# Performance work log

Measured on AMD Instinct MI355X. Metric: run time of the kernel, lower is better.

Reference implementation:

```python
import jax, jax.numpy as jnp
import numpy as np

IN_F, HID, OUT = 768, 64, 1
BATCH = 131072
NNZ1 = int(0.1 * IN_F * HID)   # 4915
NNZ2 = int(0.1 * HID * HID)    # 409
NNZ3 = int(0.5 * HID * OUT)    # 32


def _coo(key, nnz, n_rows, n_cols):
    kr, kc, kv = jax.random.split(key, 3)
    rows = jax.random.randint(kr, (nnz,), 0, n_rows, dtype=jnp.int32)
    cols = jax.random.randint(kc, (nnz,), 0, n_cols, dtype=jnp.int32)
    vals = jax.random.normal(kv, (nnz,), dtype=jnp.float32)
    return jnp.stack([rows, cols]), vals


def setup_inputs() -> dict:
    key = jax.random.key(0)
    kx, k1, k2, k3, kb1, kb2, kb3 = jax.random.split(key, 7)
    x = jax.random.normal(kx, (BATCH, IN_F), dtype=jnp.float32)
    idx1, val1 = _coo(k1, NNZ1, IN_F, HID)
    idx2, val2 = _coo(k2, NNZ2, HID, HID)
    idx3, val3 = _coo(k3, NNZ3, HID, OUT)
    b1 = jax.random.normal(kb1, (HID,), dtype=jnp.float32)
    b2 = jax.random.normal(kb2, (HID,), dtype=jnp.float32)
    b3 = jax.random.normal(kb3, (OUT,), dtype=jnp.float32)
    return {"x": x, "idx1": idx1, "val1": val1, "b1": b1,
            "idx2": idx2, "val2": val2, "b2": b2,
            "idx3": idx3, "val3": val3, "b3": b3}


def _densify(idx, vals, shape):
    # COO -> dense; duplicate indices accumulate (torch coalesce semantics)
    return jnp.zeros(shape, dtype=vals.dtype).at[idx[0], idx[1]].add(vals)


def reference(x, idx1, val1, b1, idx2, val2, b2, idx3, val3, b3):
    x = x.reshape(x.shape[0], -1)                      # [B, IN_F]
    W1 = _densify(idx1, val1, (IN_F, HID))
    W2 = _densify(idx2, val2, (HID, HID))
    W3 = _densify(idx3, val3, (HID, OUT))
    h = jax.nn.relu(x @ W1 + b1)                       # [B, 64]
    h = jax.nn.relu(h @ W2 + b2)                       # [B, 64]
    return h @ W3 + b3                                 # [B, 1]
```

## Files before the change

kernel.cpp:

```cpp
#include <hip/hip_runtime.h>
#include <cstdint>
#include <cstddef>

#define IN_F 768
#define HID  64
#define NNZ1 4915
#define NNZ2 409
#define NNZ3 32
#define BATCH 131072

#define OFF_W1D 0u
#define OFF_W2D 196608u
#define OFF_W3D 212992u
#define OFF_W1F 213248u
#define OFF_W2F 311552u
#define WS_NEED 319744u

typedef __bf16 bf16x8 __attribute__((ext_vector_type(8)));
typedef float  f32x4  __attribute__((ext_vector_type(4)));

union FragU { bf16x8 v; uint32_t u[4]; uint4 q; };

__device__ __forceinline__ uint32_t f2bf1(float f) {
    uint32_t u = __float_as_uint(f);
    return (u + 0x7FFFu + ((u >> 16) & 1u)) >> 16;
}
__device__ __forceinline__ uint32_t f2bf2(float lo, float hi) {
    uint32_t a = __float_as_uint(lo);
    uint32_t b = __float_as_uint(hi);
    a = a + 0x7FFFu + ((a >> 16) & 1u);
    b = b + 0x7FFFu + ((b >> 16) & 1u);
    return (a >> 16) | (b & 0xFFFF0000u);
}

__global__ void scatter_coo(const int* __restrict__ idx1, const float* __restrict__ val1,
                            const int* __restrict__ idx2, const float* __restrict__ val2,
                            const int* __restrict__ idx3, const float* __restrict__ val3,
                            float* __restrict__ W1d, float* __restrict__ W2d,
                            float* __restrict__ W3d) {
    int t = blockIdx.x * blockDim.x + threadIdx.x;
    if (t < NNZ1) {
        int r = idx1[t], c = idx1[NNZ1 + t];
        atomicAdd(&W1d[r * HID + c], val1[t]);
    } else if (t < NNZ1 + NNZ2) {
        int i = t - NNZ1;
        int r = idx2[i], c = idx2[NNZ2 + i];
        atomicAdd(&W2d[r * HID + c], val2[i]);
    } else if (t < NNZ1 + NNZ2 + NNZ3) {
        int i = t - NNZ1 - NNZ2;
        int r = idx3[i], c = idx3[NNZ3 + i];
        atomicAdd(&W3d[r * 1 + c], val3[i]);
    }
}

__global__ void frag_build(const float* __restrict__ W1d, const float* __restrict__ W2d,
                           uint4* __restrict__ W1f, uint4* __restrict__ W2f) {
    int t = blockIdx.x * blockDim.x + threadIdx.x;
    const int n1 = 24 * 4 * 64;
    const int n2 = 2 * 4 * 64;
    if (t < n1) {
        int lane = t & 63;
        int fi = t >> 6;
        int kstep = fi >> 2, nt = fi & 3;
        int m = lane & 15, quad = lane >> 4;
        uint32_t u[4];
#pragma unroll
        for (int jj = 0; jj < 4; ++jj) {
            int k = kstep * 32 + quad * 8 + jj * 2;
            u[jj] = f2bf2(W1d[k * HID + nt * 16 + m], W1d[(k + 1) * HID + nt * 16 + m]);
        }
        W1f[t] = make_uint4(u[0], u[1], u[2], u[3]);
    } else if (t < n1 + n2) {
        int tt = t - n1;
        int lane = tt & 63;
        int fi = tt >> 6;
        int kstep = fi >> 2, nt = fi & 3;
        int m = lane & 15, quad = lane >> 4;
        uint32_t u[4];
#pragma unroll
        for (int jj = 0; jj < 4; ++jj) {
            int k = kstep * 32 + quad * 8 + jj * 2;
            u[jj] = f2bf2(W2d[k * HID + nt * 16 + m], W2d[(k + 1) * HID + nt * 16 + m]);
        }
        W2f[tt] = make_uint4(u[0], u[1], u[2], u[3]);
    }
}

__global__ __launch_bounds__(256) void mlp_fused(
    const float* __restrict__ x,
    const uint4* __restrict__ W1f,
    const uint4* __restrict__ W2f,
    const float* __restrict__ W3d,
    const float* __restrict__ b1,
    const float* __restrict__ b2,
    const float* __restrict__ b3,
    float* __restrict__ out)
{
    __shared__ __align__(16) uint16_t h1s[4][16][72];

    const int lane = threadIdx.x & 63;
    const int w    = threadIdx.x >> 6;
    const int m    = lane & 15;
    const int quad = lane >> 4;
    const int rowbase = blockIdx.x * 64 + w * 16;

    f32x4 acc[4] = {{0,0,0,0},{0,0,0,0},{0,0,0,0},{0,0,0,0}};

    const float* xr = x + (size_t)(rowbase + m) * IN_F + quad * 8;
    const uint4* w1p = W1f + lane;

#pragma unroll 2
    for (int k = 0; k < 24; ++k) {
        const float4 xa = *(const float4*)(xr + k * 32);
        const float4 xb = *(const float4*)(xr + k * 32 + 4);
        FragU a;
        a.u[0] = f2bf2(xa.x, xa.y);
        a.u[1] = f2bf2(xa.z, xa.w);
        a.u[2] = f2bf2(xb.x, xb.y);
        a.u[3] = f2bf2(xb.z, xb.w);
        FragU b0, b1f, b2f, b3f;
        b0.q  = w1p[(k * 4 + 0) * 64];
        b1f.q = w1p[(k * 4 + 1) * 64];
        b2f.q = w1p[(k * 4 + 2) * 64];
        b3f.q = w1p[(k * 4 + 3) * 64];
        acc[0] = __builtin_amdgcn_mfma_f32_16x16x32_bf16(a.v, b0.v,  acc[0], 0, 0, 0);
        acc[1] = __builtin_amdgcn_mfma_f32_16x16x32_bf16(a.v, b1f.v, acc[1], 0, 0, 0);
        acc[2] = __builtin_amdgcn_mfma_f32_16x16x32_bf16(a.v, b2f.v, acc[2], 0, 0, 0);
        acc[3] = __builtin_amdgcn_mfma_f32_16x16x32_bf16(a.v, b3f.v, acc[3], 0, 0, 0);
    }

#pragma unroll
    for (int nt = 0; nt < 4; ++nt) {
        const int col = nt * 16 + m;
        const float bias = b1[col];
#pragma unroll
        for (int r = 0; r < 4; ++r) {
            float h = acc[nt][r] + bias;
            h = h > 0.f ? h : 0.f;
            h1s[w][quad * 4 + r][col] = (uint16_t)f2bf1(h);
        }
    }

    f32x4 acc2[4] = {{0,0,0,0},{0,0,0,0},{0,0,0,0},{0,0,0,0}};
#pragma unroll
    for (int k2 = 0; k2 < 2; ++k2) {
        FragU a2;
        a2.q = *(const uint4*)&h1s[w][m][k2 * 32 + quad * 8];
#pragma unroll
        for (int nt = 0; nt < 4; ++nt) {
            FragU bb; bb.q = W2f[(k2 * 4 + nt) * 64 + lane];
            acc2[nt] = __builtin_amdgcn_mfma_f32_16x16x32_bf16(a2.v, bb.v, acc2[nt], 0, 0, 0);
        }
    }

    float w3v[4];
#pragma unroll
    for (int nt = 0; nt < 4; ++nt) w3v[nt] = W3d[nt * 16 + m];

    float p[4] = {0.f, 0.f, 0.f, 0.f};
#pragma unroll
    for (int nt = 0; nt < 4; ++nt) {
        const float bias = b2[nt * 16 + m];
#pragma unroll
        for (int r = 0; r < 4; ++r) {
            float h = acc2[nt][r] + bias;
            h = h > 0.f ? h : 0.f;
            p[r] += h * w3v[nt];
        }
    }
#pragma unroll
    for (int off = 1; off < 16; off <<= 1) {
#pragma unroll
        for (int r = 0; r < 4; ++r) p[r] += __shfl_xor(p[r], off, 16);
    }
    const float bb3 = b3[0];
    if (m == 0) {
#pragma unroll
        for (int r = 0; r < 4; ++r) out[rowbase + quad * 4 + r] = p[r] + bb3;
    }
}

extern "C" void kernel_launch(void* const* d_in, const int* in_sizes, int n_in,
                              void* d_out, int out_size, void* d_ws, size_t ws_size,
                              hipStream_t stream) {
    const float* x    = (const float*)d_in[0];
    const int*   idx1 = (const int*)  d_in[1];
    const float* val1 = (const float*)d_in[2];
    const float* b1   = (const float*)d_in[3];
    const int*   idx2 = (const int*)  d_in[4];
    const float* val2 = (const float*)d_in[5];
    const float* b2   = (const float*)d_in[6];
    const int*   idx3 = (const int*)  d_in[7];
    const float* val3 = (const float*)d_in[8];
    const float* b3   = (const float*)d_in[9];
    float* out = (float*)d_out;

    char* ws = (char*)d_ws;
    float* W1d = (float*)(ws + OFF_W1D);
    float* W2d = (float*)(ws + OFF_W2D);
    float* W3d = (float*)(ws + OFF_W3D);
    uint4* W1f = (uint4*)(ws + OFF_W1F);
    uint4* W2f = (uint4*)(ws + OFF_W2F);

    hipMemsetAsync(d_ws, 0, OFF_W1F, stream);

    const int nnz_total = NNZ1 + NNZ2 + NNZ3;
    scatter_coo<<<(nnz_total + 255) / 256, 256, 0, stream>>>(
        idx1, val1, idx2, val2, idx3, val3, W1d, W2d, W3d);

    const int nfrag = 24 * 4 * 64 + 2 * 4 * 64;
    frag_build<<<(nfrag + 255) / 256, 256, 0, stream>>>(W1d, W2d, W1f, W2f);

    mlp_fused<<<BATCH / 64, 256, 0, stream>>>(x, W1f, W2f, W3d, b1, b2, b3, out);
}
```

Before: 555.9 us.

## Process 32 rows per wave with two-step register prefetch of x and W1

Each wave now computes two 16-row tiles, sharing each W1 fragment across both to halve weight loads per row. x and W1 fragments are loaded two k-steps ahead into double-buffered registers to hide global memory latency. The fp32-to-bf16 packing uses a vector convert builtin instead of manual rounding. Register use rises and the grid halves, which may reduce occupancy.

```diff
diff --git a/kernel.cpp b/kernel.cpp
--- a/kernel.cpp
+++ b/kernel.cpp
@@ -18,8 +18,10 @@
 
 typedef __bf16 bf16x8 __attribute__((ext_vector_type(8)));
 typedef float  f32x4  __attribute__((ext_vector_type(4)));
+typedef float  f32x8  __attribute__((ext_vector_type(8)));
 
 union FragU { bf16x8 v; uint32_t u[4]; uint4 q; };
+union F8U   { float4 f4[2]; f32x8 v8; };
 
 __device__ __forceinline__ uint32_t f2bf1(float f) {
     uint32_t u = __float_as_uint(f);
@@ -31,6 +33,11 @@
     a = a + 0x7FFFu + ((a >> 16) & 1u);
     b = b + 0x7FFFu + ((b >> 16) & 1u);
     return (a >> 16) | (b & 0xFFFF0000u);
+}
+
+__device__ __forceinline__ bf16x8 pack8(float4 a, float4 b) {
+    F8U u; u.f4[0] = a; u.f4[1] = b;
+    return __builtin_convertvector(u.v8, bf16x8);
 }
 
 __global__ void scatter_coo(const int* __restrict__ idx1, const float* __restrict__ val1,
@@ -86,7 +93,7 @@
     }
 }
 
-__global__ __launch_bounds__(256) void mlp_fused(
+__global__ __launch_bounds__(256, 4) void mlp_fused(
     const float* __restrict__ x,
     const uint4* __restrict__ W1f,
     const uint4* __restrict__ W2f,
@@ -96,37 +103,61 @@
     const float* __restrict__ b3,
     float* __restrict__ out)
 {
-    __shared__ __align__(16) uint16_t h1s[4][16][72];
+    __shared__ __align__(16) uint16_t h1s[4][32][72];
 
     const int lane = threadIdx.x & 63;
     const int w    = threadIdx.x >> 6;
     const int m    = lane & 15;
     const int quad = lane >> 4;
-    const int rowbase = blockIdx.x * 64 + w * 16;
-
-    f32x4 acc[4] = {{0,0,0,0},{0,0,0,0},{0,0,0,0},{0,0,0,0}};
-
-    const float* xr = x + (size_t)(rowbase + m) * IN_F + quad * 8;
+    const int rowbase = blockIdx.x * 128 + w * 32;
+
+    f32x4 acc0[4] = {{0,0,0,0},{0,0,0,0},{0,0,0,0},{0,0,0,0}};
+    f32x4 acc1[4] = {{0,0,0,0},{0,0,0,0},{0,0,0,0},{0,0,0,0}};
+
+    const float* xr0 = x + (size_t)(rowbase + m) * IN_F + quad * 8;
+    const float* xr1 = xr0 + (size_t)16 * IN_F;
     const uint4* w1p = W1f + lane;
+
+    float4 xa[2][4];
+    uint4  bq[2][4];
+
+#pragma unroll
+    for (int kk = 0; kk < 2; ++kk) {
+        xa[kk][0] = *(const float4*)(xr0 + kk * 32);
+        xa[kk][1] = *(const float4*)(xr0 + kk * 32 + 4);
+        xa[kk][2] = *(const float4*)(xr1 + kk * 32);
+        xa[kk][3] = *(const float4*)(xr1 + kk * 32 + 4);
+#pragma unroll
+        for (int nt = 0; nt < 4; ++nt) bq[kk][nt] = w1p[(kk * 4 + nt) * 64];
+    }
 
 #pragma unroll 2
     for (int k = 0; k < 24; ++k) {
-        const float4 xa = *(const float4*)(xr + k * 32);
-        const float4 xb = *(const float4*)(xr + k * 32 + 4);
-        FragU a;
-        a.u[0] = f2bf2(xa.x, xa.y);
-        a.u[1] = f2bf2(xa.z, xa.w);
-        a.u[2] = f2bf2(xb.x, xb.y);
-        a.u[3] = f2bf2(xb.z, xb.w);
+        const int cb = k & 1;
+        const float4 x0a = xa[cb][0], x0b = xa[cb][1];
+        const float4 x1a = xa[cb][2], x1b = xa[cb][3];
         FragU b0, b1f, b2f, b3f;
-        b0.q  = w1p[(k * 4 + 0) * 64];
-        b1f.q = w1p[(k * 4 + 1) * 64];
-        b2f.q = w1p[(k * 4 + 2) * 64];
-        b3f.q = w1p[(k * 4 + 3) * 64];
-        acc[0] = __builtin_amdgcn_mfma_f32_16x16x32_bf16(a.v, b0.v,  acc[0], 0, 0, 0);
-        acc[1] = __builtin_amdgcn_mfma_f32_16x16x32_bf16(a.v, b1f.v, acc[1], 0, 0, 0);
-        acc[2] = __builtin_amdgcn_mfma_f32_16x16x32_bf16(a.v, b2f.v, acc[2], 0, 0, 0);
-        acc[3] = __builtin_amdgcn_mfma_f32_16x16x32_bf16(a.v, b3f.v, acc[3], 0, 0, 0);
+        b0.q = bq[cb][0]; b1f.q = bq[cb][1]; b2f.q = bq[cb][2]; b3f.q = bq[cb][3];
+        if (k < 22) {
+            const int kn = k + 2;
+            xa[cb][0] = *(const float4*)(xr0 + kn * 32);
+            xa[cb][1] = *(const float4*)(xr0 + kn * 32 + 4);
+            xa[cb][2] = *(const float4*)(xr1 + kn * 32);
+            xa[cb][3] = *(const float4*)(xr1 + kn * 32 + 4);
+#pragma unroll
+            for (int nt = 0; nt < 4; ++nt) bq[cb][nt] = w1p[(kn * 4 + nt) * 64];
+        }
+        FragU a0, a1;
+        a0.v = pack8(x0a, x0b);
+        a1.v = pack8(x1a, x1b);
+        acc0[0] = __builtin_amdgcn_mfma_f32_16x16x32_bf16(a0.v, b0.v,  acc0[0], 0, 0, 0);
+        acc0[1] = __builtin_amdgcn_mfma_f32_16x16x32_bf16(a0.v, b1f.v, acc0[1], 0, 0, 0);
+        acc0[2] = __builtin_amdgcn_mfma_f32_16x16x32_bf16(a0.v, b2f.v, acc0[2], 0, 0, 0);
+        acc0[3] = __builtin_amdgcn_mfma_f32_16x16x32_bf16(a0.v, b3f.v, acc0[3], 0, 0, 0);
+        acc1[0] = __builtin_amdgcn_mfma_f32_16x16x32_bf16(a1.v, b0.v,  acc1[0], 0, 0, 0);
+        acc1[1] = __builtin_amdgcn_mfma_f32_16x16x32_bf16(a1.v, b1f.v, acc1[1], 0, 0, 0);
+        acc1[2] = __builtin_amdgcn_mfma_f32_16x16x32_bf16(a1.v, b2f.v, acc1[2], 0, 0, 0);
+        acc1[3] = __builtin_amdgcn_mfma_f32_16x16x32_bf16(a1.v, b3f.v, acc1[3], 0, 0, 0);
     }
 
 #pragma unroll
@@ -135,21 +166,27 @@
         const float bias = b1[col];
 #pragma unroll
         for (int r = 0; r < 4; ++r) {
-            float h = acc[nt][r] + bias;
-            h = h > 0.f ? h : 0.f;
-            h1s[w][quad * 4 + r][col] = (uint16_t)f2bf1(h);
-        }
-    }
-
-    f32x4 acc2[4] = {{0,0,0,0},{0,0,0,0},{0,0,0,0},{0,0,0,0}};
+            float h0 = acc0[nt][r] + bias;
+            h0 = h0 > 0.f ? h0 : 0.f;
+            h1s[w][quad * 4 + r][col] = (uint16_t)f2bf1(h0);
+            float h1 = acc1[nt][r] + bias;
+            h1 = h1 > 0.f ? h1 : 0.f;
+            h1s[w][16 + quad * 4 + r][col] = (uint16_t)f2bf1(h1);
+        }
+    }
+
+    f32x4 acc20[4] = {{0,0,0,0},{0,0,0,0},{0,0,0,0},{0,0,0,0}};
+    f32x4 acc21[4] = {{0,0,0,0},{0,0,0,0},{0,0,0,0},{0,0,0,0}};
 #pragma unroll
     for (int k2 = 0; k2 < 2; ++k2) {
-        FragU a2;
-        a2.q = *(const uint4*)&h1s[w][m][k2 * 32 + quad * 8];
+        FragU a20, a21;
+        a20.q = *(const uint4*)&h1s[w][m][k2 * 32 + quad * 8];
+        a21.q = *(const uint4*)&h1s[w][16 + m][k2 * 32 + quad * 8];
 #pragma unroll
         for (int nt = 0; nt < 4; ++nt) {
             FragU bb; bb.q = W2f[(k2 * 4 + nt) * 64 + lane];
-            acc2[nt] = __builtin_amdgcn_mfma_f32_16x16x32_bf16(a2.v, bb.v, acc2[nt], 0, 0, 0);
+            acc20[nt] = __builtin_amdgcn_mfma_f32_16x16x32_bf16(a20.v, bb.v, acc20[nt], 0, 0, 0);
+            acc21[nt] = __builtin_amdgcn_mfma_f32_16x16x32_bf16(a21.v, bb.v, acc21[nt], 0, 0, 0);
         }
     }
 
@@ -157,26 +194,36 @@
 #pragma unroll
     for (int nt = 0; nt < 4; ++nt) w3v[nt] = W3d[nt * 16 + m];
 
-    float p[4] = {0.f, 0.f, 0.f, 0.f};
+    float p0[4] = {0.f, 0.f, 0.f, 0.f};
+    float p1[4] = {0.f, 0.f, 0.f, 0.f};
 #pragma unroll
     for (int nt = 0; nt < 4; ++nt) {
         const float bias = b2[nt * 16 + m];
 #pragma unroll
         for (int r = 0; r < 4; ++r) {
-            float h = acc2[nt][r] + bias;
-            h = h > 0.f ? h : 0.f;
-            p[r] += h * w3v[nt];
+            float h0 = acc20[nt][r] + bias;
+            h0 = h0 > 0.f ? h0 : 0.f;
+            p0[r] += h0 * w3v[nt];
+            float h1 = acc21[nt][r] + bias;
+            h1 = h1 > 0.f ? h1 : 0.f;
+            p1[r] += h1 * w3v[nt];
         }
     }
 #pragma unroll
     for (int off = 1; off < 16; off <<= 1) {
 #pragma unroll
-        for (int r = 0; r < 4; ++r) p[r] += __shfl_xor(p[r], off, 16);
+        for (int r = 0; r < 4; ++r) {
+            p0[r] += __shfl_xor(p0[r], off, 16);
+            p1[r] += __shfl_xor(p1[r], off, 16);
+        }
     }
     const float bb3 = b3[0];
     if (m == 0) {
 #pragma unroll
-        for (int r = 0; r < 4; ++r) out[rowbase + quad * 4 + r] = p[r] + bb3;
+        for (int r = 0; r < 4; ++r) {
+            out[rowbase + quad * 4 + r] = p0[r] + bb3;
+            out[rowbase + 16 + quad * 4 + r] = p1[r] + bb3;
+        }
     }
 }
 
@@ -211,5 +258,5 @@
     const int nfrag = 24 * 4 * 64 + 2 * 4 * 64;
     frag_build<<<(nfrag + 255) / 256, 256, 0, stream>>>(W1d, W2d, W1f, W2f);
 
-    mlp_fused<<<BATCH / 64, 256, 0, stream>>>(x, W1f, W2f, W3d, b1, b2, b3, out);
-}
+    mlp_fused<<<BATCH / 128, 256, 0, stream>>>(x, W1f, W2f, W3d, b1, b2, b3, out);
+}
```

Result: slower. 598.0 us (+7.6%).

## Software-pipeline x loads with 64-wide K windows and permuted W1 fragments

Applied to the files above, without the earlier changes.

Each lane now loads 16 contiguous floats (64 bytes) of its x row per 64-wide K window, and two windows are prefetched into registers ahead of use. W1 fragments are rebuilt with a permuted K ordering so the split of each lane's 16 values into two bf16x8 A fragments matches the B fragments. The manual rounding is replaced by a vector convertvector to bf16. This aims to hide global-load latency in this memory-bound kernel and widen accesses, at the cost of more registers for the double-buffered x values and eight B fragments.

```diff
diff --git a/kernel.cpp b/kernel.cpp
--- a/kernel.cpp
+++ b/kernel.cpp
@@ -18,8 +18,10 @@
 
 typedef __bf16 bf16x8 __attribute__((ext_vector_type(8)));
 typedef float  f32x4  __attribute__((ext_vector_type(4)));
+typedef float  f32x8  __attribute__((ext_vector_type(8)));
 
 union FragU { bf16x8 v; uint32_t u[4]; uint4 q; };
+union F8U   { float4 f4[2]; f32x8 v8; };
 
 __device__ __forceinline__ uint32_t f2bf1(float f) {
     uint32_t u = __float_as_uint(f);
@@ -31,6 +33,11 @@
     a = a + 0x7FFFu + ((a >> 16) & 1u);
     b = b + 0x7FFFu + ((b >> 16) & 1u);
     return (a >> 16) | (b & 0xFFFF0000u);
+}
+
+__device__ __forceinline__ bf16x8 pack8(float4 a, float4 b) {
+    F8U u; u.f4[0] = a; u.f4[1] = b;
+    return __builtin_convertvector(u.v8, bf16x8);
 }
 
 __global__ void scatter_coo(const int* __restrict__ idx1, const float* __restrict__ val1,
@@ -63,10 +70,11 @@
         int fi = t >> 6;
         int kstep = fi >> 2, nt = fi & 3;
         int m = lane & 15, quad = lane >> 4;
+        int kbase = (kstep >> 1) * 64 + quad * 16 + (kstep & 1) * 8;
         uint32_t u[4];
 #pragma unroll
         for (int jj = 0; jj < 4; ++jj) {
-            int k = kstep * 32 + quad * 8 + jj * 2;
+            int k = kbase + jj * 2;
             u[jj] = f2bf2(W1d[k * HID + nt * 16 + m], W1d[(k + 1) * HID + nt * 16 + m]);
         }
         W1f[t] = make_uint4(u[0], u[1], u[2], u[3]);
@@ -106,27 +114,42 @@
 
     f32x4 acc[4] = {{0,0,0,0},{0,0,0,0},{0,0,0,0},{0,0,0,0}};
 
-    const float* xr = x + (size_t)(rowbase + m) * IN_F + quad * 8;
+    const float* xr = x + (size_t)(rowbase + m) * IN_F + quad * 16;
     const uint4* w1p = W1f + lane;
 
+    float4 xw[2][4];
+#pragma unroll
+    for (int i = 0; i < 4; ++i) {
+        xw[0][i] = *(const float4*)(xr + 0 * 64 + i * 4);
+        xw[1][i] = *(const float4*)(xr + 1 * 64 + i * 4);
+    }
+
 #pragma unroll 2
-    for (int k = 0; k < 24; ++k) {
-        const float4 xa = *(const float4*)(xr + k * 32);
-        const float4 xb = *(const float4*)(xr + k * 32 + 4);
-        FragU a;
-        a.u[0] = f2bf2(xa.x, xa.y);
-        a.u[1] = f2bf2(xa.z, xa.w);
-        a.u[2] = f2bf2(xb.x, xb.y);
-        a.u[3] = f2bf2(xb.z, xb.w);
-        FragU b0, b1f, b2f, b3f;
-        b0.q  = w1p[(k * 4 + 0) * 64];
-        b1f.q = w1p[(k * 4 + 1) * 64];
-        b2f.q = w1p[(k * 4 + 2) * 64];
-        b3f.q = w1p[(k * 4 + 3) * 64];
-        acc[0] = __builtin_amdgcn_mfma_f32_16x16x32_bf16(a.v, b0.v,  acc[0], 0, 0, 0);
-        acc[1] = __builtin_amdgcn_mfma_f32_16x16x32_bf16(a.v, b1f.v, acc[1], 0, 0, 0);
-        acc[2] = __builtin_amdgcn_mfma_f32_16x16x32_bf16(a.v, b2f.v, acc[2], 0, 0, 0);
-        acc[3] = __builtin_amdgcn_mfma_f32_16x16x32_bf16(a.v, b3f.v, acc[3], 0, 0, 0);
+    for (int win = 0; win < 12; ++win) {
+        const int cb = win & 1;
+        const float4 x0 = xw[cb][0], x1 = xw[cb][1], x2 = xw[cb][2], x3 = xw[cb][3];
+        if (win < 10) {
+#pragma unroll
+            for (int i = 0; i < 4; ++i)
+                xw[cb][i] = *(const float4*)(xr + (win + 2) * 64 + i * 4);
+        }
+        uint4 bq[8];
+#pragma unroll
+        for (int i = 0; i < 8; ++i) bq[i] = w1p[(win * 8 + i) * 64];
+
+        FragU a0, a1;
+        a0.v = pack8(x0, x1);
+        a1.v = pack8(x2, x3);
+#pragma unroll
+        for (int nt = 0; nt < 4; ++nt) {
+            FragU bb; bb.q = bq[nt];
+            acc[nt] = __builtin_amdgcn_mfma_f32_16x16x32_bf16(a0.v, bb.v, acc[nt], 0, 0, 0);
+        }
+#pragma unroll
+        for (int nt = 0; nt < 4; ++nt) {
+            FragU bb; bb.q = bq[4 + nt];
+            acc[nt] = __builtin_amdgcn_mfma_f32_16x16x32_bf16(a1.v, bb.v, acc[nt], 0, 0, 0);
+        }
     }
 
 #pragma unroll
```

Result: no change. 555.8 us (-0.0%).
